# Kernel tuning notes

Measured on AMD Instinct MI355X. Metric: run time of the kernel, lower is better.

The kernel has to match this reference:

```python
import jax, jax.numpy as jnp
import numpy as np

B, S, D, H = 4, 2048, 1024, 16
HD = D // H
NEG = -1e30


def setup_inputs() -> dict:
    key = jax.random.key(0)
    ks = jax.random.split(key, 6)
    scale = 1.0 / np.sqrt(D)
    return {
        "q": jax.random.normal(ks[0], (B, S, D), jnp.float32),
        "k": jax.random.normal(ks[1], (B, S, D), jnp.float32),
        "v": jax.random.normal(ks[2], (B, S, D), jnp.float32),
        "mask": jnp.ones((B, 1, S), jnp.float32),
        "wq": jax.random.normal(ks[3], (D, D), jnp.float32) * scale,
        "bq": jnp.zeros((D,), jnp.float32),
        "wk": jax.random.normal(ks[4], (D, D), jnp.float32) * scale,
        "bk": jnp.zeros((D,), jnp.float32),
        "wv": jax.random.normal(ks[5], (D, D), jnp.float32) * scale,
        "bv": jnp.zeros((D,), jnp.float32),
    }


def _heads(x):
    # (B,S,D) -> (B,H,S,HD)
    return x.reshape(B, S, H, HD).transpose(0, 2, 1, 3)


def reference(q, k, v, mask, wq, bq, wk, bk, wv, bv):
    # pointwise Conv1D(kernel=1) == linear: x @ W^T + b (W: (out,in))
    qh = _heads(jnp.einsum('bsd,ed->bse', q, wq) + bq)
    kh = _heads(jnp.einsum('bsd,ed->bse', k, wk) + bk)
    vh = _heads(jnp.einsum('bsd,ed->bse', v, wv) + bv)
    scores = jnp.einsum('bhqd,bhkd->bhqk', qh, kh) / jnp.sqrt(jnp.float32(HD))
    # mask_logits: x + (1 - mask) * -1e30, mask (B,1,S) -> (B,1,1,S)
    scores = scores + (1.0 - mask[:, None, :, :]) * NEG
    probs = jax.nn.softmax(scores, axis=-1)  # dropout is identity in eval
    ctx = jnp.einsum('bhqk,bhkd->bhqd', probs, vh)
    return ctx.transpose(0, 2, 1, 3).reshape(B, S, D)
```

## Files before the change

kernel.cpp:

```cpp
#include <hip/hip_runtime.h>
#include <math.h>

typedef __attribute__((ext_vector_type(8)))  _Float16 f16x8;
typedef __attribute__((ext_vector_type(4)))  _Float16 f16x4;
typedef __attribute__((ext_vector_type(2)))  __fp16   h16x2;
typedef __attribute__((ext_vector_type(4)))  float    f32x4;
typedef __attribute__((ext_vector_type(16))) float    f32x16;
typedef unsigned int u32;

static constexpr int B  = 4;
static constexpr int S  = 2048;
static constexpr int D  = 1024;
static constexpr int H  = 16;
static constexpr int HD = 64;

union U64cvt { f16x4 h; ushort4 u; };
union W4 { u32 w[4]; f16x8 v; };

__device__ __forceinline__ void gld16(const void* g, void* l) {
    __builtin_amdgcn_global_load_lds((const u32*)g, (u32*)l, 16, 0, 0);
}

__global__ __launch_bounds__(256)
void proj_qkv(const float* __restrict__ qi, const float* __restrict__ ki,
              const float* __restrict__ vi,
              const float* __restrict__ wqp, const float* __restrict__ wkp,
              const float* __restrict__ wvp,
              const float* __restrict__ bqp, const float* __restrict__ bkp,
              const float* __restrict__ bvp,
              unsigned short* __restrict__ ws)
{
    const int bid = blockIdx.x;
    const int wg  = (bid & 7) * 192 + (bid >> 3);
    const int z   = wg >> 9;
    const int rem = wg & 511;
    const int m0  = (rem >> 3) * 128;
    const int n0  = (rem & 7) * 128;

    const float* A    = (z == 0) ? qi  : (z == 1) ? ki  : vi;
    const float* W    = (z == 0) ? wqp : (z == 1) ? wkp : wvp;
    const float* bias = (z == 0) ? bqp : (z == 1) ? bkp : bvp;
    unsigned short* out = ws + (size_t)z * ((size_t)B * S * D);

    const int tid  = threadIdx.x;
    const int lane = tid & 63;
    const int wid  = tid >> 6;
    const int wr   = wid >> 1;
    const int wc   = wid & 1;

    __shared__ __align__(16) unsigned char lA[2][8192];
    __shared__ __align__(16) unsigned char lB[2][8192];

    f32x4 acc[4][4];
#pragma unroll
    for (int i = 0; i < 4; ++i)
#pragma unroll
        for (int j = 0; j < 4; ++j) acc[i][j] = (f32x4){0.f, 0.f, 0.f, 0.f};

    const int rb = (lane >> 4) * 16;

    int srow[4], sc4[4], soff[4];
#pragma unroll
    for (int i = 0; i < 4; ++i) {
        const int f = tid + 256 * i;
        srow[i] = f >> 3;
        sc4[i]  = f & 7;
        soff[i] = ((f >> 3) * 64 + (f & 7) * 8) ^ ((((f >> 3)) & 7) << 4);
    }

#pragma unroll
    for (int i = 0; i < 4; ++i) {
        const float4 va = *(const float4*)(A + (size_t)(m0 + srow[i]) * D + sc4[i] * 4);
        const float4 vw = *(const float4*)(W + (size_t)(n0 + srow[i]) * D + sc4[i] * 4);
        U64cvt ua, uw;
        ua.h = (f16x4){(_Float16)va.x, (_Float16)va.y, (_Float16)va.z, (_Float16)va.w};
        uw.h = (f16x4){(_Float16)vw.x, (_Float16)vw.y, (_Float16)vw.z, (_Float16)vw.w};
        *(ushort4*)(lA[0] + soff[i]) = ua.u;
        *(ushort4*)(lB[0] + soff[i]) = uw.u;
    }
    __syncthreads();

    for (int kt = 0; kt < 32; ++kt) {
        const int cb = kt & 1, nx = cb ^ 1;

        f16x8 af[4], bf[4];
#pragma unroll
        for (int mi = 0; mi < 4; ++mi) {
            const int row = wr * 64 + mi * 16 + (lane & 15);
            af[mi] = *(const f16x8*)(lA[cb] + ((row * 64 + rb) ^ ((row & 7) << 4)));
        }
#pragma unroll
        for (int ni = 0; ni < 4; ++ni) {
            const int row = wc * 64 + ni * 16 + (lane & 15);
            bf[ni] = *(const f16x8*)(lB[cb] + ((row * 64 + rb) ^ ((row & 7) << 4)));
        }

        float4 pva[4], pvw[4];
        if (kt < 31) {
            const int k0n = (kt + 1) * 32;
#pragma unroll
            for (int i = 0; i < 4; ++i) {
                pva[i] = *(const float4*)(A + (size_t)(m0 + srow[i]) * D + k0n + sc4[i] * 4);
                pvw[i] = *(const float4*)(W + (size_t)(n0 + srow[i]) * D + k0n + sc4[i] * 4);
            }
        }

        __builtin_amdgcn_s_setprio(1);
#pragma unroll
        for (int mi = 0; mi < 4; ++mi)
#pragma unroll
            for (int ni = 0; ni < 4; ++ni)
                acc[mi][ni] = __builtin_amdgcn_mfma_f32_16x16x32_f16(af[mi], bf[ni], acc[mi][ni], 0, 0, 0);
        __builtin_amdgcn_s_setprio(0);

        if (kt < 31) {
#pragma unroll
            for (int i = 0; i < 4; ++i) {
                U64cvt ua, uw;
                ua.h = (f16x4){(_Float16)pva[i].x, (_Float16)pva[i].y, (_Float16)pva[i].z, (_Float16)pva[i].w};
                uw.h = (f16x4){(_Float16)pvw[i].x, (_Float16)pvw[i].y, (_Float16)pvw[i].z, (_Float16)pvw[i].w};
                *(ushort4*)(lA[nx] + soff[i]) = ua.u;
                *(ushort4*)(lB[nx] + soff[i]) = uw.u;
            }
        }
        __syncthreads();
    }

#pragma unroll
    for (int mi = 0; mi < 4; ++mi) {
        const int gmBase = m0 + wr * 64 + mi * 16 + ((lane >> 4) << 2);
        const int b  = gmBase >> 11;
        const int s0 = gmBase & 2047;
        const int tV   = s0 >> 6;
        const int kv6  = s0 & 63;
        const int ksg  = kv6 >> 4;
        const int hi2v = (kv6 >> 3) & 1;
        const int jb   = kv6 & 7;
#pragma unroll
        for (int ni = 0; ni < 4; ++ni) {
            const int gn = n0 + wc * 64 + ni * 16 + (lane & 15);
            const float bb = bias[gn];
            const int hh = gn >> 6;
            const int hd = gn & 63;
            const size_t bhbase = ((size_t)b * H + hh) * ((size_t)S * HD);
            if (z == 0) {
#pragma unroll
                for (int r = 0; r < 4; ++r) {
                    const int gm = gmBase + r;
                    const _Float16 hv = (_Float16)(acc[mi][ni][r] + bb);
                    out[bhbase + (size_t)(gm & 2047) * HD + hd] =
                        __builtin_bit_cast(unsigned short, hv);
                }
            } else if (z == 1) {
                const int ks   = hd >> 4;
                const int hi2k = (hd >> 3) & 1;
                const int j    = hd & 7;
#pragma unroll
                for (int r = 0; r < 4; ++r) {
                    const int s = (gmBase + r) & 2047;
                    const int t = s >> 6;
                    const int q = ((s >> 5) & 1) * 4 + ks;
                    const _Float16 hv = (_Float16)(acc[mi][ni][r] + bb);
                    out[bhbase + (((size_t)t * 8 + q) * 64 + hi2k * 32 + (s & 31)) * 8 + j] =
                        __builtin_bit_cast(unsigned short, hv);
                }
            } else {
                const int nb  = hd >> 5;
                const int c31 = hd & 31;
                const int q   = nb * 4 + ksg;
                U64cvt uu;
#pragma unroll
                for (int r = 0; r < 4; ++r)
                    uu.h[r] = (_Float16)(acc[mi][ni][r] + bb);
                *(ushort4*)(out + bhbase +
                    (((size_t)tV * 8 + q) * 64 + hi2v * 32 + c31) * 8 + jb) = uu.u;
            }
        }
    }
}

__global__ __launch_bounds__(256)
void attn_f16(const unsigned short* __restrict__ qh,
              const unsigned short* __restrict__ kf,
              const unsigned short* __restrict__ vf,
              const float* __restrict__ mask,
              float* __restrict__ out)
{
    const int flat = blockIdx.y * gridDim.x + blockIdx.x;
    const int sw   = (flat & 7) * 128 + (flat >> 3);
    const int bh   = sw >> 4;
    const int q0   = (sw & 15) * 128;

    const int b = bh >> 4;
    const int h = bh & 15;
    const unsigned short* Q  = qh + (size_t)bh * S * HD;
    const unsigned short* KF = kf + (size_t)bh * S * HD;
    const unsigned short* VF = vf + (size_t)bh * S * HD;

    const int tid  = threadIdx.x;
    const int lane = tid & 63;
    const int wid  = tid >> 6;
    const int l31  = lane & 31;
    const int hi2  = lane >> 5;

    __shared__ __align__(16) unsigned char Kl[2][8192];
    __shared__ __align__(16) unsigned char Vl[2][8192];
    __shared__ __align__(16) float maskb[2][64];

    const int ldsA = wid * 1024;
    const int ldsB = wid * 1024 + 4096;
    const int g0   = tid * 8;
    const int g1   = tid * 8 + 2048;

    const float C = 0.18033688011112042f;
    const float SHIFT = -5.770780163555854f;

    f16x8 aq[4];
    {
        const unsigned short* qrow = Q + (size_t)(q0 + wid * 32 + l31) * HD;
#pragma unroll
        for (int ks = 0; ks < 4; ++ks)
            aq[ks] = *(const f16x8*)(qrow + ks * 16 + hi2 * 8);
    }

    float ls0 = 0.f, ls1 = 0.f;
    f32x16 accO[2];
    accO[0] = (f32x16){};
    accO[1] = (f32x16){};
    const h16x2 one2 = {(__fp16)1.0f, (__fp16)1.0f};

    gld16(KF + g0, Kl[0] + ldsA);
    gld16(KF + g1, Kl[0] + ldsB);
    gld16(VF + g0, Vl[0] + ldsA);
    gld16(VF + g1, Vl[0] + ldsB);
    if (tid < 64)
        maskb[0][tid] = fmaf(1.0f - mask[(size_t)b * S + tid], -1.4426950408889634e30f, SHIFT);
    __syncthreads();

    const int lane16 = lane * 16;
    for (int t = 0; t < S / 64; ++t) {
        const int cb = t & 1, nx = cb ^ 1;
        const unsigned char* Kc = Kl[cb];
        const unsigned char* Vc = Vl[cb];

        f32x16 p[2];
        p[0] = (f32x16){};
        p[1] = (f32x16){};
        __builtin_amdgcn_s_setprio(1);
#pragma unroll
        for (int kb = 0; kb < 2; ++kb)
#pragma unroll
            for (int ks = 0; ks < 4; ++ks) {
                const f16x8 ak = *(const f16x8*)(Kc + lane16 + (kb * 4 + ks) * 1024);
                p[kb] = __builtin_amdgcn_mfma_f32_32x32x16_f16(ak, aq[ks], p[kb], 0, 0, 0);
            }
        __builtin_amdgcn_s_setprio(0);

        if (t < S / 64 - 1) {
            const int nt = (t + 1) * 4096;
            gld16(KF + nt + g0, Kl[nx] + ldsA);
            gld16(KF + nt + g1, Kl[nx] + ldsB);
            gld16(VF + nt + g0, Vl[nx] + ldsA);
            gld16(VF + nt + g1, Vl[nx] + ldsB);
            if (tid < 64)
                maskb[nx][tid] = fmaf(1.0f - mask[(size_t)b * S + (t + 1) * 64 + tid],
                                      -1.4426950408889634e30f, SHIFT);
        }

        f16x8 pa[4];
#pragma unroll
        for (int kb = 0; kb < 2; ++kb) {
            float pe[16];
#pragma unroll
            for (int g = 0; g < 4; ++g) {
                const f32x4 mg = *(const f32x4*)(&maskb[cb][kb * 32 + g * 8 + hi2 * 4]);
#pragma unroll
                for (int e = 0; e < 4; ++e)
                    pe[g * 4 + e] = exp2f(fmaf(p[kb][g * 4 + e], C, mg[e]));
            }
#pragma unroll
            for (int ks2 = 0; ks2 < 2; ++ks2) {
                const int o = ks2 * 8;
                const h16x2 h0 = __builtin_amdgcn_cvt_pkrtz(pe[o + 0], pe[o + 1]);
                const h16x2 h1 = __builtin_amdgcn_cvt_pkrtz(pe[o + 2], pe[o + 3]);
                const h16x2 h2 = __builtin_amdgcn_cvt_pkrtz(pe[o + 4], pe[o + 5]);
                const h16x2 h3 = __builtin_amdgcn_cvt_pkrtz(pe[o + 6], pe[o + 7]);
                ls0 = __builtin_amdgcn_fdot2(h0, one2, ls0, false);
                ls1 = __builtin_amdgcn_fdot2(h1, one2, ls1, false);
                ls0 = __builtin_amdgcn_fdot2(h2, one2, ls0, false);
                ls1 = __builtin_amdgcn_fdot2(h3, one2, ls1, false);
                u32 a0 = __builtin_bit_cast(u32, h0);
                u32 a1 = __builtin_bit_cast(u32, h1);
                u32 a2 = __builtin_bit_cast(u32, h2);
                u32 a3 = __builtin_bit_cast(u32, h3);
                asm volatile("v_permlane32_swap_b32 %0, %1" : "+v"(a0), "+v"(a2));
                asm volatile("v_permlane32_swap_b32 %0, %1" : "+v"(a1), "+v"(a3));
                W4 w;
                w.w[0] = a0; w.w[1] = a1; w.w[2] = a2; w.w[3] = a3;
                pa[kb * 2 + ks2] = w.v;
            }
        }

        __builtin_amdgcn_s_setprio(1);
#pragma unroll
        for (int nb = 0; nb < 2; ++nb)
#pragma unroll
            for (int ksg = 0; ksg < 4; ++ksg) {
                const f16x8 bv = *(const f16x8*)(Vc + lane16 + (nb * 4 + ksg) * 1024);
                accO[nb] = __builtin_amdgcn_mfma_f32_32x32x16_f16(pa[ksg], bv, accO[nb], 0, 0, 0);
            }
        __builtin_amdgcn_s_setprio(0);

        __syncthreads();
    }

    float lsum = ls0 + ls1;
    lsum += __shfl_xor(lsum, 32);
    const float linv = 1.0f / lsum;

    float lr[16];
#pragma unroll
    for (int r = 0; r < 16; ++r)
        lr[r] = __shfl(linv, (r & 3) + 8 * (r >> 2) + 4 * hi2);

#pragma unroll
    for (int nb = 0; nb < 2; ++nb) {
        const int dcol = h * HD + nb * 32 + l31;
#pragma unroll
        for (int r = 0; r < 16; ++r) {
            const int qrow = q0 + wid * 32 + (r & 3) + 8 * (r >> 2) + 4 * hi2;
            out[((size_t)b * S + qrow) * D + dcol] = accO[nb][r] * lr[r];
        }
    }
}

extern "C" void kernel_launch(void* const* d_in, const int* in_sizes, int n_in,
                              void* d_out, int out_size, void* d_ws, size_t ws_size,
                              hipStream_t stream)
{
    const float* q    = (const float*)d_in[0];
    const float* k    = (const float*)d_in[1];
    const float* v    = (const float*)d_in[2];
    const float* mask = (const float*)d_in[3];
    const float* wq   = (const float*)d_in[4];
    const float* bq   = (const float*)d_in[5];
    const float* wk   = (const float*)d_in[6];
    const float* bk   = (const float*)d_in[7];
    const float* wv   = (const float*)d_in[8];
    const float* bv   = (const float*)d_in[9];

    unsigned short* ws = (unsigned short*)d_ws;
    const size_t per = (size_t)B * S * D;

    proj_qkv<<<1536, 256, 0, stream>>>(q, k, v, wq, wk, wv, bq, bk, bv, ws);

    dim3 ga(S / 128, B * H);
    attn_f16<<<ga, 256, 0, stream>>>(ws, ws + per, ws + 2 * per, mask, (float*)d_out);
}
```

Baseline: 229.2 us.

## Prefetch projection tiles two steps ahead with 16-byte packed fp16 LDS writes

Restructures the QKV projection GEMM's global-to-LDS pipeline. Global loads are now issued two k-steps ahead and held in registers, and converting and storing tile k+1 into LDS happens at the start of each iteration instead of after the MFMAs. Each thread now handles 8 contiguous floats, converts them with packed round-toward-zero conversions, and writes one 16-byte LDS store instead of two 8-byte ones. Load latency gets more time to hide, at the cost of more live registers and a switch from round-to-nearest to round-toward-zero for the fp16 cast.

```diff
diff --git a/kernel.cpp b/kernel.cpp
--- a/kernel.cpp
+++ b/kernel.cpp
@@ -19,6 +19,15 @@
 
 __device__ __forceinline__ void gld16(const void* g, void* l) {
     __builtin_amdgcn_global_load_lds((const u32*)g, (u32*)l, 16, 0, 0);
+}
+
+__device__ __forceinline__ void cvtwr16(const float4& x, const float4& y, void* dst) {
+    W4 w;
+    w.w[0] = __builtin_bit_cast(u32, __builtin_amdgcn_cvt_pkrtz(x.x, x.y));
+    w.w[1] = __builtin_bit_cast(u32, __builtin_amdgcn_cvt_pkrtz(x.z, x.w));
+    w.w[2] = __builtin_bit_cast(u32, __builtin_amdgcn_cvt_pkrtz(y.x, y.y));
+    w.w[3] = __builtin_bit_cast(u32, __builtin_amdgcn_cvt_pkrtz(y.z, y.w));
+    *(f16x8*)dst = w.v;
 }
 
 __global__ __launch_bounds__(256)
@@ -59,29 +68,42 @@
 
     const int rb = (lane >> 4) * 16;
 
-    int srow[4], sc4[4], soff[4];
-#pragma unroll
-    for (int i = 0; i < 4; ++i) {
+    int srow[2], sc8[2], soff[2];
+#pragma unroll
+    for (int i = 0; i < 2; ++i) {
         const int f = tid + 256 * i;
-        srow[i] = f >> 3;
-        sc4[i]  = f & 7;
-        soff[i] = ((f >> 3) * 64 + (f & 7) * 8) ^ ((((f >> 3)) & 7) << 4);
-    }
-
-#pragma unroll
-    for (int i = 0; i < 4; ++i) {
-        const float4 va = *(const float4*)(A + (size_t)(m0 + srow[i]) * D + sc4[i] * 4);
-        const float4 vw = *(const float4*)(W + (size_t)(n0 + srow[i]) * D + sc4[i] * 4);
-        U64cvt ua, uw;
-        ua.h = (f16x4){(_Float16)va.x, (_Float16)va.y, (_Float16)va.z, (_Float16)va.w};
-        uw.h = (f16x4){(_Float16)vw.x, (_Float16)vw.y, (_Float16)vw.z, (_Float16)vw.w};
-        *(ushort4*)(lA[0] + soff[i]) = ua.u;
-        *(ushort4*)(lB[0] + soff[i]) = uw.u;
+        srow[i] = f >> 2;
+        sc8[i]  = f & 3;
+        soff[i] = ((f >> 2) * 64 + (f & 3) * 16) ^ ((((f >> 2)) & 7) << 4);
+    }
+
+#pragma unroll
+    for (int i = 0; i < 2; ++i) {
+        const float* pa = A + (size_t)(m0 + srow[i]) * D + sc8[i] * 8;
+        const float* pw = W + (size_t)(n0 + srow[i]) * D + sc8[i] * 8;
+        cvtwr16(*(const float4*)pa, *(const float4*)(pa + 4), lA[0] + soff[i]);
+        cvtwr16(*(const float4*)pw, *(const float4*)(pw + 4), lB[0] + soff[i]);
+    }
+    float4 pa0[2], pa1[2], pw0[2], pw1[2];
+#pragma unroll
+    for (int i = 0; i < 2; ++i) {
+        const float* pa = A + (size_t)(m0 + srow[i]) * D + 32 + sc8[i] * 8;
+        const float* pw = W + (size_t)(n0 + srow[i]) * D + 32 + sc8[i] * 8;
+        pa0[i] = *(const float4*)pa;  pa1[i] = *(const float4*)(pa + 4);
+        pw0[i] = *(const float4*)pw;  pw1[i] = *(const float4*)(pw + 4);
     }
     __syncthreads();
 
     for (int kt = 0; kt < 32; ++kt) {
         const int cb = kt & 1, nx = cb ^ 1;
+
+        if (kt < 31) {
+#pragma unroll
+            for (int i = 0; i < 2; ++i) {
+                cvtwr16(pa0[i], pa1[i], lA[nx] + soff[i]);
+                cvtwr16(pw0[i], pw1[i], lB[nx] + soff[i]);
+            }
+        }
 
         f16x8 af[4], bf[4];
 #pragma unroll
@@ -95,13 +117,14 @@
             bf[ni] = *(const f16x8*)(lB[cb] + ((row * 64 + rb) ^ ((row & 7) << 4)));
         }
 
-        float4 pva[4], pvw[4];
-        if (kt < 31) {
-            const int k0n = (kt + 1) * 32;
-#pragma unroll
-            for (int i = 0; i < 4; ++i) {
-                pva[i] = *(const float4*)(A + (size_t)(m0 + srow[i]) * D + k0n + sc4[i] * 4);
-                pvw[i] = *(const float4*)(W + (size_t)(n0 + srow[i]) * D + k0n + sc4[i] * 4);
+        if (kt < 30) {
+            const int k2 = (kt + 2) * 32;
+#pragma unroll
+            for (int i = 0; i < 2; ++i) {
+                const float* pa = A + (size_t)(m0 + srow[i]) * D + k2 + sc8[i] * 8;
+                const float* pw = W + (size_t)(n0 + srow[i]) * D + k2 + sc8[i] * 8;
+                pa0[i] = *(const float4*)pa;  pa1[i] = *(const float4*)(pa + 4);
+                pw0[i] = *(const float4*)pw;  pw1[i] = *(const float4*)(pw + 4);
             }
         }
 
@@ -113,16 +136,6 @@
                 acc[mi][ni] = __builtin_amdgcn_mfma_f32_16x16x32_f16(af[mi], bf[ni], acc[mi][ni], 0, 0, 0);
         __builtin_amdgcn_s_setprio(0);
 
-        if (kt < 31) {
-#pragma unroll
-            for (int i = 0; i < 4; ++i) {
-                U64cvt ua, uw;
-                ua.h = (f16x4){(_Float16)pva[i].x, (_Float16)pva[i].y, (_Float16)pva[i].z, (_Float16)pva[i].w};
-                uw.h = (f16x4){(_Float16)pvw[i].x, (_Float16)pvw[i].y, (_Float16)pvw[i].z, (_Float16)pvw[i].w};
-                *(ushort4*)(lA[nx] + soff[i]) = ua.u;
-                *(ushort4*)(lB[nx] + soff[i]) = uw.u;
-            }
-        }
         __syncthreads();
     }
 
```

New measurement: 229.6 us. No clear change (+0.2%).
